# Performance work log

Hardware: AMD Instinct MI355X
Metric: run time of the kernel (lower is better)

Reference implementation:

```python
import jax, jax.numpy as jnp
import numpy as np

WS = (7, 7, 7)
NUM_HEADS = 16
DIM = 512
HEAD_DIM = DIM // NUM_HEADS
SCALE = HEAD_DIM ** (-0.5)


def _rel_index():
    # Swin-3D relative position index, computed statically with numpy.
    coords = np.stack(np.meshgrid(np.arange(WS[0]), np.arange(WS[1]), np.arange(WS[2]), indexing='ij'))
    coords = coords.reshape(3, -1)                       # [3, n]
    rel = coords[:, :, None] - coords[:, None, :]        # [3, n, n]
    rel = rel.transpose(1, 2, 0).astype(np.int64)        # [n, n, 3]
    rel[..., 0] += WS[0] - 1
    rel[..., 1] += WS[1] - 1
    rel[..., 2] += WS[2] - 1
    rel[..., 0] *= (2 * WS[1] - 1) * (2 * WS[2] - 1)
    rel[..., 1] *= 2 * WS[2] - 1
    return rel.sum(-1)                                   # [n, n]

REL_INDEX = jnp.asarray(_rel_index(), dtype=jnp.int32)


def setup_inputs() -> dict:
    key = jax.random.key(0)
    ks = jax.random.split(key, 6)
    B, nw = 2, 64
    b, n, c = B * nw, WS[0] * WS[1] * WS[2], DIM  # 128, 343, 512
    x = jax.random.normal(ks[0], (b, n, c), jnp.float32)
    q_global = jax.random.normal(ks[1], (B, 1, NUM_HEADS, n, HEAD_DIM), jnp.float32)
    mask = jax.random.normal(ks[2], (nw, n, n), jnp.float32)
    kv_w = jax.random.normal(ks[3], (2 * c, c), jnp.float32) * (c ** -0.5)
    proj_w = jax.random.normal(ks[4], (c, c), jnp.float32) * (c ** -0.5)
    proj_b = jnp.zeros((c,), jnp.float32)
    num_rel = (2 * WS[0] - 1) * (2 * WS[1] - 1) * (2 * WS[2] - 1)  # 2197
    rpb_table = jax.random.normal(ks[5], (num_rel, NUM_HEADS), jnp.float32) * 0.02
    return {"x": x, "D": 7, "H": 7, "W": 7, "mask": mask, "q_global": q_global,
            "kv_w": kv_w, "proj_w": proj_w, "proj_b": proj_b, "rpb_table": rpb_table}


def reference(x, D, H, W, mask, q_global, kv_w, proj_w, proj_b, rpb_table):
    b, n, c = x.shape
    h, hd = NUM_HEADS, c // NUM_HEADS
    B = q_global.shape[0]
    # q_global [B,1,h,n,hd] repeated over windows -> [b,h,n,hd]
    q = jnp.broadcast_to(q_global, (B, b // B, h, n, hd)).reshape(b, h, n, hd) * SCALE
    kv = (x @ kv_w.T).reshape(b, n, 2, h, hd).transpose(2, 0, 3, 1, 4)  # [2,b,h,n,hd]
    k, v = kv[0], kv[1]
    attn = jnp.einsum('bhnd,bhmd->bhnm', q, k)  # [b,h,n,n]
    bias = rpb_table[REL_INDEX[:n, :n].reshape(-1)].reshape(n, n, h).transpose(2, 0, 1)
    attn = attn + bias[None]
    nw = mask.shape[0]
    attn = (attn.reshape(b // nw, nw, h, n, n) + mask[None, :, None]).reshape(b, h, n, n)
    attn = jax.nn.softmax(attn, axis=-1)
    out = jnp.einsum('bhnm,bhmd->bhnd', attn, v).transpose(0, 2, 1, 3).reshape(b, n, c)
    return out @ proj_w.T + proj_b
```

## Files before the change

kernel.cpp:

```cpp
#include <hip/hip_runtime.h>

typedef __bf16 bf16x8 __attribute__((ext_vector_type(8)));
typedef __bf16 bf16x2 __attribute__((ext_vector_type(2)));
typedef float f32x4 __attribute__((ext_vector_type(4)));
typedef unsigned u32x4v __attribute__((ext_vector_type(4)));

#define MFMA16(a, b, c) __builtin_amdgcn_mfma_f32_16x16x32_bf16(a, b, c, 0, 0, 0)
#define LOG2E 1.4426950408889634f

typedef __attribute__((address_space(3))) void lds_void;
typedef __attribute__((address_space(1))) const void gbl_void;
__device__ inline void glds16(const __bf16* g, __bf16* l) {
  __builtin_amdgcn_global_load_lds((gbl_void*)g, (lds_void*)l, 16, 0, 0);
}

__device__ inline unsigned pk2(float a, float b) {
  bf16x2 t; t[0] = (__bf16)a; t[1] = (__bf16)b;
  return __builtin_bit_cast(unsigned, t);
}

__global__ void cvt_scale(const float* __restrict__ src, __bf16* __restrict__ dst,
                          int n8, float scale) {
  int i = blockIdx.x * blockDim.x + threadIdx.x;
  if (i >= n8) return;
  const float4* p = (const float4*)(src + i * 8);
  float4 a = p[0], b = p[1];
  bf16x8 r;
  r[0] = (__bf16)(a.x * scale); r[1] = (__bf16)(a.y * scale);
  r[2] = (__bf16)(a.z * scale); r[3] = (__bf16)(a.w * scale);
  r[4] = (__bf16)(b.x * scale); r[5] = (__bf16)(b.y * scale);
  r[6] = (__bf16)(b.z * scale); r[7] = (__bf16)(b.w * scale);
  *(bf16x8*)(dst + i * 8) = r;
}

__global__ void pack_bias(const float* __restrict__ rpb, __bf16* __restrict__ dst) {
  int i = blockIdx.x * blockDim.x + threadIdx.x;
  if (i >= 16 * 15488) return;
  int h = i / 15488, rem = i % 15488;
  int qt = rem / 704, rem2 = rem % 704;
  int c = rem2 / 64, rem3 = rem2 % 64;
  int half = rem3 >> 5, qd = (rem3 >> 4) & 1, l15 = rem3 & 15;
  int key = c * 32 + (l15 >> 2) * 8 + (l15 & 3) + half * 4;
  bf16x8 v;
#pragma unroll
  for (int e = 0; e < 8; e++) {
    int q = qt * 16 + qd * 8 + e;
    float val = -1e30f;
    if (q < 343 && key < 343) {
      int q0 = q / 49, q1 = (q / 7) % 7, q2 = q % 7;
      int k0 = key / 49, k1 = (key / 7) % 7, k2 = key % 7;
      int idx = ((q0 - k0 + 6) * 13 + (q1 - k1 + 6)) * 13 + (q2 - k2 + 6);
      val = rpb[idx * 16 + h] * LOG2E;
    }
    v[e] = (__bf16)val;
  }
  *(bf16x8*)(dst + i * 8) = v;
}

__global__ void pack_mask(const float* __restrict__ mask, __bf16* __restrict__ dst) {
  int i = blockIdx.x * blockDim.x + threadIdx.x;
  if (i >= 64 * 15488) return;
  int w = i / 15488, rem = i % 15488;
  int qt = rem / 704, rem2 = rem % 704;
  int c = rem2 / 64, rem3 = rem2 % 64;
  int half = rem3 >> 5, qd = (rem3 >> 4) & 1, l15 = rem3 & 15;
  int key = c * 32 + (l15 >> 2) * 8 + (l15 & 3) + half * 4;
  const float* s = mask + w * 117649;
  bf16x8 v;
#pragma unroll
  for (int e = 0; e < 8; e++) {
    int q = qt * 16 + qd * 8 + e;
    float val = (q < 343 && key < 343) ? s[q * 343 + key] * LOG2E : -1e30f;
    v[e] = (__bf16)val;
  }
  *(bf16x8*)(dst + i * 8) = v;
}

template <int MODE>
__global__ void __launch_bounds__(256, 2)
gemm_async(const void* __restrict__ Araw, const __bf16* __restrict__ B, const int K,
           void* __restrict__ out0, void* __restrict__ out1,
           const float* __restrict__ pbias) {
  __shared__ __bf16 As[128 * 32];
  __shared__ __bf16 Bs[128 * 32];
  const int tid = threadIdx.x;
  const int lane = tid & 63, wave = tid >> 6;
  const int quad = lane >> 4, l15 = lane & 15;
  const int wm = wave >> 1, wn = wave & 1;
  const int nwg = gridDim.x * gridDim.y;
  int bid = blockIdx.y * gridDim.x + blockIdx.x;
  {
    const int xcd = bid & 7, idx = bid >> 3, qq = nwg >> 3, rr = nwg & 7;
    bid = (xcd < rr ? xcd * (qq + 1) : rr * (qq + 1) + (xcd - rr) * qq) + idx;
  }
  const int m0 = (bid / gridDim.x) * 128, n0 = (bid % gridDim.x) * 128;
  const int sr = lane >> 2, sc = (lane & 3) * 8;
  const __bf16* Bb = B + (n0 + wave * 16 + sr) * K + sc;
  __bf16* Bsl = Bs + wave * 512;
  const __bf16* Ab = nullptr; const float* Af = nullptr;
  __bf16* Asl = As + wave * 512;
  if constexpr (MODE == 0) {
    Af = (const float*)Araw + (size_t)(m0 + wave * 16 + sr) * K + sc;
  } else {
    Ab = (const __bf16*)Araw + (size_t)(m0 + wave * 16 + sr) * K + sc;
  }
  f32x4 acc[4][4] = {};
  for (int k0 = 0; k0 < K; k0 += 32) {
    if constexpr (MODE == 0) {
      float4 a0 = *(const float4*)(Af + k0), a1 = *(const float4*)(Af + k0 + 4);
      float4 b0 = *(const float4*)(Af + (size_t)64 * K + k0);
      float4 b1 = *(const float4*)(Af + (size_t)64 * K + k0 + 4);
      bf16x8 c0, c1;
      c0[0] = (__bf16)a0.x; c0[1] = (__bf16)a0.y; c0[2] = (__bf16)a0.z; c0[3] = (__bf16)a0.w;
      c0[4] = (__bf16)a1.x; c0[5] = (__bf16)a1.y; c0[6] = (__bf16)a1.z; c0[7] = (__bf16)a1.w;
      c1[0] = (__bf16)b0.x; c1[1] = (__bf16)b0.y; c1[2] = (__bf16)b0.z; c1[3] = (__bf16)b0.w;
      c1[4] = (__bf16)b1.x; c1[5] = (__bf16)b1.y; c1[6] = (__bf16)b1.z; c1[7] = (__bf16)b1.w;
      *(bf16x8*)(As + (wave * 16 + sr) * 32 + sc) = c0;
      *(bf16x8*)(As + (64 + wave * 16 + sr) * 32 + sc) = c1;
    } else {
      glds16(Ab + k0, Asl);
      glds16(Ab + 64 * K + k0, Asl + 2048);
    }
    glds16(Bb + k0, Bsl);
    glds16(Bb + 64 * K + k0, Bsl + 2048);
    __syncthreads();
    bf16x8 af[4], bfr[4];
#pragma unroll
    for (int i = 0; i < 4; i++) {
      af[i] = *(const bf16x8*)(As + (wm * 64 + i * 16 + l15) * 32 + quad * 8);
      bfr[i] = *(const bf16x8*)(Bs + (wn * 64 + i * 16 + l15) * 32 + quad * 8);
    }
#pragma unroll
    for (int i = 0; i < 4; i++)
#pragma unroll
      for (int j = 0; j < 4; j++)
        acc[i][j] = MFMA16(af[i], bfr[j], acc[i][j]);
    __syncthreads();
  }
#pragma unroll
  for (int i = 0; i < 4; i++) {
    const int rowb = m0 + wm * 64 + i * 16 + quad * 4;
#pragma unroll
    for (int r = 0; r < 4; r++) {
      const int row = rowb + r;
      if constexpr (MODE == 0) {
        const int bb = row / 343, pos = row % 343;
#pragma unroll
        for (int j = 0; j < 4; j++) {
          const int col = n0 + wn * 64 + j * 16 + l15;
          const int two = col >> 9, hh = (col >> 5) & 15, d = col & 31;
          __bf16* dst = two ? (__bf16*)out1 : (__bf16*)out0;
          dst[((bb * 16 + hh) * 343 + pos) * 32 + d] = (__bf16)acc[i][j][r];
        }
      } else {
        float* o = (float*)out0;
#pragma unroll
        for (int j = 0; j < 4; j++) {
          const int col = n0 + wn * 64 + j * 16 + l15;
          o[row * 512 + col] = acc[i][j][r] + pbias[col];
        }
      }
    }
  }
}

__global__ void __launch_bounds__(512, 4)
attn_win(const __bf16* __restrict__ qs, const __bf16* __restrict__ kk,
         const __bf16* __restrict__ vv, const __bf16* __restrict__ bias_pk,
         const __bf16* __restrict__ mask_pk, __bf16* __restrict__ ao) {
  __shared__ __bf16 Ks[352 * 40];
  __shared__ __bf16 Vt[32 * 360];
  const int bid = blockIdx.x;
  const int bh = (bid & 7) * 256 + (bid >> 3);
  const int b = bh >> 4, h = bh & 15;
  const int tid = threadIdx.x;
  const int lane = tid & 63, wave = tid >> 6;
  const int quad = lane >> 4, l15 = lane & 15;
  const __bf16* ksrc = kk + (b * 16 + h) * 10976;
  const __bf16* vsrc = vv + (b * 16 + h) * 10976;
  for (int i = tid; i < 352 * 4; i += 512) {
    const int row = i >> 2, seg = (i & 3) * 8;
    bf16x8 val;
    if (row < 343) {
      val = *(const bf16x8*)(ksrc + row * 32 + seg);
    } else {
#pragma unroll
      for (int e = 0; e < 8; e++) val[e] = (__bf16)0.f;
    }
    *(bf16x8*)(Ks + row * 40 + seg) = val;
  }
  Vt[(tid >> 4) * 360 + 343 + (tid & 15)] = (__bf16)0.f;
  for (int i = tid; i < 1372; i += 512) {
    const int pos = i >> 2, seg = (i & 3) * 8;
    bf16x8 v = *(const bf16x8*)(vsrc + pos * 32 + seg);
#pragma unroll
    for (int e = 0; e < 8; e++) Vt[(seg + e) * 360 + pos] = v[e];
  }

  const int b2 = b >> 6, w = b & 63;
  const __bf16* qbase = qs + (b2 * 16 + h) * 10976;
  const __bf16* tab = (quad < 2 ? bias_pk + h * 123904 : mask_pk + w * 123904)
                      + (quad & 1) * 128 + l15 * 8;
  const int nqt = (wave < 6) ? 3 : 2;

  bf16x8 aq[3];
#pragma unroll
  for (int t = 0; t < 3; t++) {
    int qt = wave + 8 * t; if (qt > 21) qt = 21;
    const int arow = qt * 16 + l15;
    const int arowc = arow < 343 ? arow : 342;
    aq[t] = *(const bf16x8*)(qbase + arowc * 32 + quad * 8);
  }
  bf16x8 ones;
  bf16x8 idf;
  {
    const __bf16 ov = (l15 == 0) ? (__bf16)1.f : (__bf16)0.f;
#pragma unroll
    for (int e = 0; e < 8; e++) {
      ones[e] = ov;
      idf[e] = ((quad & 1) * 8 + e == l15) ? (__bf16)1.f : (__bf16)0.f;
    }
  }
  const int krow = (l15 >> 2) * 8 + (l15 & 3);
  __syncthreads();

  f32x4 o0[3], o1[3], o2[3];
#pragma unroll
  for (int t = 0; t < 3; t++)
#pragma unroll
    for (int r = 0; r < 4; r++) { o0[t][r] = 0.f; o1[t][r] = 0.f; o2[t][r] = 0.f; }

  for (int c = 0; c < 11; c++) {
    const bf16x8 bk0 = *(const bf16x8*)(Ks + (c * 32 + krow) * 40 + quad * 8);
    const bf16x8 bk1 = *(const bf16x8*)(Ks + (c * 32 + krow + 4) * 40 + quad * 8);
    const bf16x8 bv0 = *(const bf16x8*)(Vt + l15 * 360 + c * 32 + quad * 8);
    const bf16x8 bv1 = *(const bf16x8*)(Vt + (16 + l15) * 360 + c * 32 + quad * 8);
#pragma unroll
    for (int t = 0; t < 3; t++) {
      if (t >= nqt) break;
      const int qt = wave + 8 * t;
      const __bf16* tb = tab + (qt * 11 + c) * 512;
      const bf16x8 f0 = *(const bf16x8*)tb;
      const bf16x8 f1 = *(const bf16x8*)(tb + 256);
      const f32x4 z = {0.f, 0.f, 0.f, 0.f};
      __builtin_amdgcn_s_setprio(1);
      f32x4 s0 = MFMA16(f0, idf, z);
      f32x4 s1 = MFMA16(f1, idf, z);
      s0 = MFMA16(bk0, aq[t], s0);
      s1 = MFMA16(bk1, aq[t], s1);
#pragma unroll
      for (int r = 0; r < 4; r++) {
        s0[r] = __builtin_amdgcn_exp2f(s0[r]);
        s1[r] = __builtin_amdgcn_exp2f(s1[r]);
      }
      u32x4v uv;
      uv[0] = pk2(s0[0], s0[1]); uv[1] = pk2(s0[2], s0[3]);
      uv[2] = pk2(s1[0], s1[1]); uv[3] = pk2(s1[2], s1[3]);
      const bf16x8 ap = __builtin_bit_cast(bf16x8, uv);
      o0[t] = MFMA16(ap, bv0, o0[t]);
      o1[t] = MFMA16(ap, bv1, o1[t]);
      o2[t] = MFMA16(ap, ones, o2[t]);
      __builtin_amdgcn_s_setprio(0);
    }
  }

#pragma unroll
  for (int t = 0; t < 3; t++) {
    if (t >= nqt) break;
    const int qt = wave + 8 * t;
#pragma unroll
    for (int r = 0; r < 4; r++) {
      const float lsum = __shfl(o2[t][r], lane & 48);
      const float inv = __builtin_amdgcn_rcpf(lsum);
      const int row = qt * 16 + quad * 4 + r;
      if (row < 343) {
        __bf16* op = ao + (b * 343 + row) * 512 + h * 32;
        op[l15] = (__bf16)(o0[t][r] * inv);
        op[16 + l15] = (__bf16)(o1[t][r] * inv);
      }
    }
  }
}

extern "C" void kernel_launch(void* const* d_in, const int* in_sizes, int n_in,
                              void* d_out, int out_size, void* d_ws, size_t ws_size,
                              hipStream_t stream) {
  (void)in_sizes; (void)n_in; (void)out_size; (void)ws_size;
  const float* x      = (const float*)d_in[0];
  const float* mask   = (const float*)d_in[4];
  const float* qg     = (const float*)d_in[5];
  const float* kv_w   = (const float*)d_in[6];
  const float* proj_w = (const float*)d_in[7];
  const float* proj_b = (const float*)d_in[8];
  const float* rpb    = (const float*)d_in[9];

  char* ws = (char*)d_ws;
  __bf16* q_bf    = (__bf16*)(ws);
  __bf16* bias_pk = (__bf16*)(ws + 702464);
  __bf16* mask_pk = (__bf16*)(ws + 4667392);
  __bf16* kvw_b   = (__bf16*)(ws + 20527104);
  __bf16* projw_b = (__bf16*)(ws + 21575680);
  __bf16* kb      = (__bf16*)(ws + 22099968);
  __bf16* vb      = (__bf16*)(ws + 67057664);
  __bf16* aob     = (__bf16*)(ws + 112015360);

  const float QSCALE = 0.17677669529663687f * LOG2E;

  cvt_scale<<<172, 256, 0, stream>>>(qg, q_bf, 43904, QSCALE);
  cvt_scale<<<256, 256, 0, stream>>>(kv_w, kvw_b, 65536, 1.f);
  cvt_scale<<<128, 256, 0, stream>>>(proj_w, projw_b, 32768, 1.f);
  pack_bias<<<968, 256, 0, stream>>>(rpb, bias_pk);
  pack_mask<<<3872, 256, 0, stream>>>(mask, mask_pk);
  gemm_async<0><<<dim3(8, 343), 256, 0, stream>>>(x, kvw_b, 512, kb, vb, nullptr);
  attn_win<<<2048, 512, 0, stream>>>(q_bf, kb, vb, bias_pk, mask_pk, aob);
  gemm_async<1><<<dim3(4, 343), 256, 0, stream>>>(aob, projw_b, 512, d_out, nullptr, proj_b);
}
```

Measured before the change: 400.9 us.

## Double K-step per iteration and register-prefetch fp32 A tile in GEMM

The GEMM main loop now handles 64 K-elements per iteration, staging two 32-wide slices in doubled LDS buffers, so it hits half as many barriers. In the fp32-input mode, the next iteration's A tile is loaded into registers while the current MFMAs run, which hides global latency behind compute. The cost is doubled LDS use (32 KB per block) and more registers for the prefetch, which may lower occupancy under the 2-blocks-per-CU launch bound. K must be a multiple of 64.

```diff
diff --git a/kernel.cpp b/kernel.cpp
--- a/kernel.cpp
+++ b/kernel.cpp
@@ -81,8 +81,8 @@
 gemm_async(const void* __restrict__ Araw, const __bf16* __restrict__ B, const int K,
            void* __restrict__ out0, void* __restrict__ out1,
            const float* __restrict__ pbias) {
-  __shared__ __bf16 As[128 * 32];
-  __shared__ __bf16 Bs[128 * 32];
+  __shared__ __bf16 As[2 * 128 * 32];
+  __shared__ __bf16 Bs[2 * 128 * 32];
   const int tid = threadIdx.x;
   const int lane = tid & 63, wave = tid >> 6;
   const int quad = lane >> 4, l15 = lane & 15;
@@ -105,36 +105,69 @@
     Ab = (const __bf16*)Araw + (size_t)(m0 + wave * 16 + sr) * K + sc;
   }
   f32x4 acc[4][4] = {};
-  for (int k0 = 0; k0 < K; k0 += 32) {
+  float4 pa[8];
+  if constexpr (MODE == 0) {
+#pragma unroll
+    for (int s = 0; s < 2; s++) {
+      pa[s * 4 + 0] = *(const float4*)(Af + s * 32);
+      pa[s * 4 + 1] = *(const float4*)(Af + s * 32 + 4);
+      pa[s * 4 + 2] = *(const float4*)(Af + (size_t)64 * K + s * 32);
+      pa[s * 4 + 3] = *(const float4*)(Af + (size_t)64 * K + s * 32 + 4);
+    }
+  }
+  for (int k0 = 0; k0 < K; k0 += 64) {
+#pragma unroll
+    for (int s = 0; s < 2; s++) {
+      glds16(Bb + k0 + s * 32, Bsl + s * 4096);
+      glds16(Bb + 64 * K + k0 + s * 32, Bsl + s * 4096 + 2048);
+    }
     if constexpr (MODE == 0) {
-      float4 a0 = *(const float4*)(Af + k0), a1 = *(const float4*)(Af + k0 + 4);
-      float4 b0 = *(const float4*)(Af + (size_t)64 * K + k0);
-      float4 b1 = *(const float4*)(Af + (size_t)64 * K + k0 + 4);
-      bf16x8 c0, c1;
-      c0[0] = (__bf16)a0.x; c0[1] = (__bf16)a0.y; c0[2] = (__bf16)a0.z; c0[3] = (__bf16)a0.w;
-      c0[4] = (__bf16)a1.x; c0[5] = (__bf16)a1.y; c0[6] = (__bf16)a1.z; c0[7] = (__bf16)a1.w;
-      c1[0] = (__bf16)b0.x; c1[1] = (__bf16)b0.y; c1[2] = (__bf16)b0.z; c1[3] = (__bf16)b0.w;
-      c1[4] = (__bf16)b1.x; c1[5] = (__bf16)b1.y; c1[6] = (__bf16)b1.z; c1[7] = (__bf16)b1.w;
-      *(bf16x8*)(As + (wave * 16 + sr) * 32 + sc) = c0;
-      *(bf16x8*)(As + (64 + wave * 16 + sr) * 32 + sc) = c1;
+#pragma unroll
+      for (int s = 0; s < 2; s++) {
+        const float4 a0 = pa[s * 4 + 0], a1 = pa[s * 4 + 1];
+        const float4 b0 = pa[s * 4 + 2], b1 = pa[s * 4 + 3];
+        bf16x8 c0, c1;
+        c0[0] = (__bf16)a0.x; c0[1] = (__bf16)a0.y; c0[2] = (__bf16)a0.z; c0[3] = (__bf16)a0.w;
+        c0[4] = (__bf16)a1.x; c0[5] = (__bf16)a1.y; c0[6] = (__bf16)a1.z; c0[7] = (__bf16)a1.w;
+        c1[0] = (__bf16)b0.x; c1[1] = (__bf16)b0.y; c1[2] = (__bf16)b0.z; c1[3] = (__bf16)b0.w;
+        c1[4] = (__bf16)b1.x; c1[5] = (__bf16)b1.y; c1[6] = (__bf16)b1.z; c1[7] = (__bf16)b1.w;
+        *(bf16x8*)(As + s * 4096 + (wave * 16 + sr) * 32 + sc) = c0;
+        *(bf16x8*)(As + s * 4096 + (64 + wave * 16 + sr) * 32 + sc) = c1;
+      }
     } else {
-      glds16(Ab + k0, Asl);
-      glds16(Ab + 64 * K + k0, Asl + 2048);
-    }
-    glds16(Bb + k0, Bsl);
-    glds16(Bb + 64 * K + k0, Bsl + 2048);
+#pragma unroll
+      for (int s = 0; s < 2; s++) {
+        glds16(Ab + k0 + s * 32, Asl + s * 4096);
+        glds16(Ab + 64 * K + k0 + s * 32, Asl + s * 4096 + 2048);
+      }
+    }
     __syncthreads();
-    bf16x8 af[4], bfr[4];
-#pragma unroll
-    for (int i = 0; i < 4; i++) {
-      af[i] = *(const bf16x8*)(As + (wm * 64 + i * 16 + l15) * 32 + quad * 8);
-      bfr[i] = *(const bf16x8*)(Bs + (wn * 64 + i * 16 + l15) * 32 + quad * 8);
-    }
-#pragma unroll
-    for (int i = 0; i < 4; i++)
-#pragma unroll
-      for (int j = 0; j < 4; j++)
-        acc[i][j] = MFMA16(af[i], bfr[j], acc[i][j]);
+    if constexpr (MODE == 0) {
+      if (k0 + 64 < K) {
+        const float* An = Af + k0 + 64;
+#pragma unroll
+        for (int s = 0; s < 2; s++) {
+          pa[s * 4 + 0] = *(const float4*)(An + s * 32);
+          pa[s * 4 + 1] = *(const float4*)(An + s * 32 + 4);
+          pa[s * 4 + 2] = *(const float4*)(An + (size_t)64 * K + s * 32);
+          pa[s * 4 + 3] = *(const float4*)(An + (size_t)64 * K + s * 32 + 4);
+        }
+      }
+    }
+#pragma unroll
+    for (int s = 0; s < 2; s++) {
+      bf16x8 af[4], bfr[4];
+#pragma unroll
+      for (int i = 0; i < 4; i++) {
+        af[i] = *(const bf16x8*)(As + s * 4096 + (wm * 64 + i * 16 + l15) * 32 + quad * 8);
+        bfr[i] = *(const bf16x8*)(Bs + s * 4096 + (wn * 64 + i * 16 + l15) * 32 + quad * 8);
+      }
+#pragma unroll
+      for (int i = 0; i < 4; i++)
+#pragma unroll
+        for (int j = 0; j < 4; j++)
+          acc[i][j] = MFMA16(af[i], bfr[j], acc[i][j]);
+    }
     __syncthreads();
   }
 #pragma unroll
```

New measurement: 399.1 us. Within noise of the previous version (-0.4%).
